# Kernel tuning notes

Hardware: AMD Instinct MI355X
Metric: run time of the kernel (lower is better)

## Reference

```python
import jax, jax.numpy as jnp
import numpy as np

N, T, K, C, O = 2048, 20, 32, 32, 64  # agents, timesteps, neighbors, in_ch, out_ch


def setup_inputs() -> dict:
    key = jax.random.key(0)
    ks = jax.random.split(key, 8)
    s = 0.05
    x = jax.random.normal(ks[0], (N, T, C), dtype=jnp.float32)
    A = jax.random.randint(ks[1], (T, N, K), 0, N)  # neighbor indices into agent dim
    conv_w = jax.random.normal(ks[2], (O, C), jnp.float32) * s  # 1x1 conv == linear [O,C]
    conv_b = jax.random.normal(ks[3], (O,), jnp.float32) * s
    w_ih = jax.random.normal(ks[4], (4 * O, O), jnp.float32) * s  # LSTM gates i,f,g,o
    w_hh = jax.random.normal(ks[5], (4 * O, O), jnp.float32) * s
    b_ih = jax.random.normal(ks[6], (4 * O,), jnp.float32) * s
    b_hh = jax.random.normal(ks[7], (4 * O,), jnp.float32) * s
    return dict(x=x, A=A, conv_w=conv_w, conv_b=conv_b,
                w_ih=w_ih, w_hh=w_hh, b_ih=b_ih, b_hh=b_hh)


def reference(x, A, conv_w, conv_b, w_ih, w_hh, b_ih, b_hh):
    n = x.shape[0]
    xt = jnp.transpose(x, (1, 0, 2))  # [T, N, C]
    # align == 1: per-timestep neighbor gather and relative difference
    gathered = jax.vmap(lambda xs, idx: xs[idx])(xt, A)  # [T, N, K, C]
    diff = gathered - xt[:, :, None, :]  # [T, N, K, C]
    # 1x1 conv (pointwise linear over channels)
    y = jnp.einsum('tnkc,oc->tnko', diff, conv_w) + conv_b  # [T, N, K, O]
    # AdaptiveMaxPool2d((seq_len, 1)): max over the neighbor axis K
    feat = jnp.max(y, axis=2)  # [T, N, O] -- LSTM input (time-major)

    h0 = jnp.zeros((n, O), jnp.float32)
    c0 = jnp.zeros((n, O), jnp.float32)

    def step(carry, x_t):
        h, c = carry
        g = x_t @ w_ih.T + h @ w_hh.T + (b_ih + b_hh)  # [N, 4O]
        i_g, f_g, g_g, o_g = jnp.split(g, 4, axis=-1)
        c = jax.nn.sigmoid(f_g) * c + jax.nn.sigmoid(i_g) * jnp.tanh(g_g)
        h = jax.nn.sigmoid(o_g) * jnp.tanh(c)
        return (h, c), h

    (hN, cN), hs = jax.lax.scan(step, (h0, c0), feat)
    out = jnp.transpose(hs, (1, 0, 2))  # [N, T, O]
    # state_tuple permuted to batch-first as in the torch module
    return out, hN[:, None, :], cN[:, None, :]
```

## Files before the change

kernel.cpp:

```cpp
#include <hip/hip_runtime.h>
#include <hip/hip_bf16.h>
#include <math.h>

#define NA 2048
#define TT 20
#define KK 32
#define CC 32
#define OO 64
#define GG 256

typedef __attribute__((ext_vector_type(8))) short short8;
typedef __attribute__((ext_vector_type(4))) float float4v;

__device__ __forceinline__ float fast_rcp(float x) {
    return __builtin_amdgcn_rcpf(x);
}
__device__ __forceinline__ float sigm(float x) {
    return fast_rcp(1.f + __expf(-x));
}
__device__ __forceinline__ float tanh_fast(float x) {
    return 1.f - 2.f * fast_rcp(1.f + __expf(2.f * x));
}
__device__ __forceinline__ unsigned cvt_rne(float f) {
    unsigned u = __float_as_uint(f);
    return (u + 0x7FFFu + ((u >> 16) & 1u)) >> 16;
}
__device__ __forceinline__ unsigned pack2(float a, float b) {
    return cvt_rne(a) | (cvt_rne(b) << 16);
}
__device__ __forceinline__ float bf_lo(unsigned u) {
    return __uint_as_float(u << 16);
}
__device__ __forceinline__ float bf_hi(unsigned u) {
    return __uint_as_float(u & 0xffff0000u);
}

__global__ __launch_bounds__(256) void proj_kernel(
    const float* __restrict__ x, const float* __restrict__ conv_w,
    const float* __restrict__ conv_b, const float* __restrict__ w_ih,
    const float* __restrict__ w_hh, const float* __restrict__ b_ih,
    const float* __restrict__ b_hh,
    __hip_bfloat16* __restrict__ P, unsigned short* __restrict__ wihb,
    unsigned short* __restrict__ whhb, float* __restrict__ biasT)
{
    const int tid = threadIdx.x;
    if (blockIdx.x == 0) {
        for (int e = tid; e < 4 * OO * OO; e += 256) {
            wihb[e] = (unsigned short)cvt_rne(w_ih[e]);
            whhb[e] = (unsigned short)cvt_rne(w_hh[e]);
        }
        float bj = b_ih[tid] + b_hh[tid];
        #pragma unroll
        for (int o = 0; o < OO; o += 4) {
            float4 cb = *(const float4*)(conv_b + o);
            float4 wr = *(const float4*)(w_ih + (size_t)tid * OO + o);
            bj = fmaf(cb.x, wr.x, bj); bj = fmaf(cb.y, wr.y, bj);
            bj = fmaf(cb.z, wr.z, bj); bj = fmaf(cb.w, wr.w, bj);
        }
        biasT[tid] = bj;
        return;
    }
    const int lane = tid & 63;
    const int wv = tid >> 6;
    float w[CC];
    #pragma unroll
    for (int c = 0; c < CC; c += 4) {
        float4 v = *(const float4*)(conv_w + lane * CC + c);
        w[c] = v.x; w[c + 1] = v.y; w[c + 2] = v.z; w[c + 3] = v.w;
    }
    const int rbase = (blockIdx.x - 1) * 16 + wv * 4;
    #pragma unroll
    for (int i = 0; i < 4; ++i) {
        int r = rbase + i;
        const float* xr = x + (size_t)r * CC;
        float a0 = 0.f, a1 = 0.f;
        #pragma unroll
        for (int c = 0; c < CC; c += 8) {
            float4 v = *(const float4*)(xr + c);
            float4 u = *(const float4*)(xr + c + 4);
            a0 = fmaf(v.x, w[c], a0);     a0 = fmaf(v.y, w[c + 1], a0);
            a0 = fmaf(v.z, w[c + 2], a0); a0 = fmaf(v.w, w[c + 3], a0);
            a1 = fmaf(u.x, w[c + 4], a1); a1 = fmaf(u.y, w[c + 5], a1);
            a1 = fmaf(u.z, w[c + 6], a1); a1 = fmaf(u.w, w[c + 7], a1);
        }
        int n = r / TT;
        int t = r - n * TT;
        ((unsigned short*)P)[(((size_t)t << 11) + n) * OO + lane] =
            (unsigned short)cvt_rne(a0 + a1);
    }
}

__global__ __launch_bounds__(256, 4) void gather_kernel(
    const __hip_bfloat16* __restrict__ P, const int* __restrict__ A,
    unsigned* __restrict__ featw)
{
    __shared__ int A_sh[4][128];
    const int tid = threadIdx.x;
    const int lane = tid & 63;
    const int wv = tid >> 6;
    const int bs = (blockIdx.x & 7) * 320 + (blockIdx.x >> 3);
    const int r0 = bs << 4;
    const int t = r0 >> 11;
    const unsigned short* Pt = (const unsigned short*)P + ((size_t)t << 17);

    const int rw = r0 + wv * 4;
    ((int2*)A_sh[wv])[lane] = ((const int2*)(A + ((size_t)rw << 5)))[lane];

    const int i_row = lane >> 4;
    const int oc8 = lane & 15;
    const char* plane = (const char*)Pt + oc8 * 8;
    const int* myA = &A_sh[wv][i_row * 32];

    const int nself = (rw + i_row) & (NA - 1);
    const uint2 su = *(const uint2*)(plane + ((size_t)nself << 7));

    float m0 = -INFINITY, m1 = -INFINITY, m2 = -INFINITY, m3 = -INFINITY;
    #pragma unroll
    for (int bb = 0; bb < 2; ++bb) {
        int idx[16];
        #pragma unroll
        for (int g = 0; g < 16; ++g)
            idx[g] = myA[bb * 16 + g];
        uint2 uv[16];
        #pragma unroll
        for (int g = 0; g < 16; ++g)
            uv[g] = *(const uint2*)(plane + ((size_t)idx[g] << 7));
        #pragma unroll
        for (int g = 0; g < 16; ++g) {
            m0 = fmaxf(m0, bf_lo(uv[g].x)); m1 = fmaxf(m1, bf_hi(uv[g].x));
            m2 = fmaxf(m2, bf_lo(uv[g].y)); m3 = fmaxf(m3, bf_hi(uv[g].y));
        }
    }
    uint2 pk;
    pk.x = pack2(m0 - bf_lo(su.x), m1 - bf_hi(su.x));
    pk.y = pack2(m2 - bf_lo(su.y), m3 - bf_hi(su.y));
    *(uint2*)&featw[((size_t)(rw + i_row) << 5) + oc8 * 2] = pk;
}

__global__ __launch_bounds__(256, 2) void lstm_kernel(
    const unsigned short* __restrict__ feat,
    const unsigned short* __restrict__ wihb,
    const unsigned short* __restrict__ whhb,
    const float* __restrict__ biasT, float* __restrict__ out)
{
    const int tid = threadIdx.x;
    const int lane = tid & 63;
    const int wv = tid >> 6;
    const int l15 = lane & 15;
    const int q = lane >> 4;
    const int a0 = blockIdx.x * 16;
    const int a = tid >> 4;
    const int c0 = (tid & 15) * 4;

    short8 bfI[4][2], bfH[4][2];
    #pragma unroll
    for (int tt2 = 0; tt2 < 4; ++tt2) {
        int row = wv * 64 + tt2 * 16 + l15;
        #pragma unroll
        for (int ks = 0; ks < 2; ++ks) {
            bfI[tt2][ks] =
                *(const short8*)(wihb + ((size_t)row << 6) + ks * 32 + q * 8);
            bfH[tt2][ks] =
                *(const short8*)(whhb + ((size_t)row << 6) + ks * 32 + q * 8);
        }
    }
    float4 bias4[4];
    #pragma unroll
    for (int g = 0; g < 4; ++g)
        bias4[g] = *(const float4*)(biasT + g * 64 + c0);

    __shared__ __align__(16) unsigned short h_sh[16 * 72];
    __shared__ float gp[4][16][68];

    {
        uint2 z; z.x = 0u; z.y = 0u;
        *(uint2*)&h_sh[a * 72 + c0] = z;
    }
    float cst[4] = {0.f, 0.f, 0.f, 0.f};

    short8 ff[2];
    #pragma unroll
    for (int ks = 0; ks < 2; ++ks)
        ff[ks] = *(const short8*)(
            feat + (((size_t)a0 + l15) << 6) + ks * 32 + q * 8);

    for (int t = 0; t < TT; ++t) {
        __syncthreads();

        float4v acc[4] = {{0.f, 0.f, 0.f, 0.f}, {0.f, 0.f, 0.f, 0.f},
                          {0.f, 0.f, 0.f, 0.f}, {0.f, 0.f, 0.f, 0.f}};
        #pragma unroll
        for (int ks = 0; ks < 2; ++ks) {
            short8 ah = *(const short8*)(&h_sh[l15 * 72 + ks * 32 + q * 8]);
            #pragma unroll
            for (int tt2 = 0; tt2 < 4; ++tt2) {
                acc[tt2] = __builtin_amdgcn_mfma_f32_16x16x32_bf16(
                    ff[ks], bfI[tt2][ks], acc[tt2], 0, 0, 0);
                acc[tt2] = __builtin_amdgcn_mfma_f32_16x16x32_bf16(
                    ah, bfH[tt2][ks], acc[tt2], 0, 0, 0);
            }
        }
        #pragma unroll
        for (int tt2 = 0; tt2 < 4; ++tt2)
            #pragma unroll
            for (int rg = 0; rg < 4; ++rg)
                gp[wv][q * 4 + rg][tt2 * 16 + l15] = acc[tt2][rg];

        short8 ffn[2];
        int tn = (t + 1 < TT) ? t + 1 : t;
        #pragma unroll
        for (int ks = 0; ks < 2; ++ks)
            ffn[ks] = *(const short8*)(
                feat + ((((size_t)tn << 11) + a0 + l15) << 6) + ks * 32 + q * 8);
        __syncthreads();

        float4 gv0 = *(const float4*)&gp[0][a][c0];
        float4 gv1 = *(const float4*)&gp[1][a][c0];
        float4 gv2 = *(const float4*)&gp[2][a][c0];
        float4 gv3 = *(const float4*)&gp[3][a][c0];
        float hv[4];
        {
            float gi[4] = {gv0.x + bias4[0].x, gv0.y + bias4[0].y,
                           gv0.z + bias4[0].z, gv0.w + bias4[0].w};
            float gf[4] = {gv1.x + bias4[1].x, gv1.y + bias4[1].y,
                           gv1.z + bias4[1].z, gv1.w + bias4[1].w};
            float gz[4] = {gv2.x + bias4[2].x, gv2.y + bias4[2].y,
                           gv2.z + bias4[2].z, gv2.w + bias4[2].w};
            float go[4] = {gv3.x + bias4[3].x, gv3.y + bias4[3].y,
                           gv3.z + bias4[3].z, gv3.w + bias4[3].w};
            #pragma unroll
            for (int e = 0; e < 4; ++e) {
                float ig = sigm(gi[e]);
                float fg = sigm(gf[e]);
                float zg = tanh_fast(gz[e]);
                float og = sigm(go[e]);
                cst[e] = fmaf(fg, cst[e], ig * zg);
                hv[e] = og * tanh_fast(cst[e]);
            }
        }
        {
            uint2 pk;
            pk.x = pack2(hv[0], hv[1]);
            pk.y = pack2(hv[2], hv[3]);
            *(uint2*)&h_sh[a * 72 + c0] = pk;
        }
        float4 ho; ho.x = hv[0]; ho.y = hv[1]; ho.z = hv[2]; ho.w = hv[3];
        *(float4*)(out + (((size_t)(a0 + a) * TT + t) << 6) + c0) = ho;
        if (t == TT - 1) {
            size_t hb = (size_t)NA * TT * OO;
            *(float4*)(out + hb + ((size_t)(a0 + a) << 6) + c0) = ho;
            float4 co; co.x = cst[0]; co.y = cst[1]; co.z = cst[2]; co.w = cst[3];
            *(float4*)(out + hb + ((size_t)NA << 6) + ((size_t)(a0 + a) << 6) + c0) = co;
        }
        ff[0] = ffn[0]; ff[1] = ffn[1];
    }
}

extern "C" void kernel_launch(void* const* d_in, const int* in_sizes, int n_in,
                              void* d_out, int out_size, void* d_ws, size_t ws_size,
                              hipStream_t stream) {
    const float* x      = (const float*)d_in[0];
    const int*   A      = (const int*)  d_in[1];
    const float* conv_w = (const float*)d_in[2];
    const float* conv_b = (const float*)d_in[3];
    const float* w_ih   = (const float*)d_in[4];
    const float* w_hh   = (const float*)d_in[5];
    const float* b_ih   = (const float*)d_in[6];
    const float* b_hh   = (const float*)d_in[7];
    float* out = (float*)d_out;

    char* ws = (char*)d_ws;
    __hip_bfloat16* P  = (__hip_bfloat16*)ws;
    size_t offF = (size_t)TT * NA * OO * 2;
    unsigned* featw = (unsigned*)(ws + offF);
    size_t offW = offF + (size_t)TT * NA * OO * 2;
    unsigned short* wihb = (unsigned short*)(ws + offW);
    unsigned short* whhb = wihb + 4 * OO * OO;
    float* biasT = (float*)(whhb + 4 * OO * OO);

    hipLaunchKernelGGL(proj_kernel, dim3(NA * TT / 16 + 1), dim3(256), 0, stream,
                       x, conv_w, conv_b, w_ih, w_hh, b_ih, b_hh,
                       P, wihb, whhb, biasT);
    hipLaunchKernelGGL(gather_kernel, dim3(NA * TT / 16), dim3(256), 0, stream,
                       P, A, featw);
    hipLaunchKernelGGL(lstm_kernel, dim3(NA / 16), dim3(256), 0, stream,
                       (const unsigned short*)featw, wihb, whhb, biasT, out);
}
```

Measured before the change: 129.0 us.

## Fuse neighbor gather-max into LSTM kernel with software-pipelined prefetch

Removes the separate gather kernel and its feature buffer: the LSTM kernel now gathers neighbor projections for step t+1 while computing step t, with features and neighbor indices double-buffered in shared memory. This avoids one launch and a global write and read of the feature tensor. The cost is that the gather work now runs on only 128 blocks instead of 2560, so it may extend the serial LSTM loop if its latency is not hidden, and register pressure rises.

New measurement: 149.3 us. 15.8% more time.

```diff
diff --git a/kernel.cpp b/kernel.cpp
--- a/kernel.cpp
+++ b/kernel.cpp
@@ -90,55 +90,8 @@
     }
 }
 
-__global__ __launch_bounds__(256, 4) void gather_kernel(
+__global__ __launch_bounds__(256, 2) void lstm_fused_kernel(
     const __hip_bfloat16* __restrict__ P, const int* __restrict__ A,
-    unsigned* __restrict__ featw)
-{
-    __shared__ int A_sh[4][128];
-    const int tid = threadIdx.x;
-    const int lane = tid & 63;
-    const int wv = tid >> 6;
-    const int bs = (blockIdx.x & 7) * 320 + (blockIdx.x >> 3);
-    const int r0 = bs << 4;
-    const int t = r0 >> 11;
-    const unsigned short* Pt = (const unsigned short*)P + ((size_t)t << 17);
-
-    const int rw = r0 + wv * 4;
-    ((int2*)A_sh[wv])[lane] = ((const int2*)(A + ((size_t)rw << 5)))[lane];
-
-    const int i_row = lane >> 4;
-    const int oc8 = lane & 15;
-    const char* plane = (const char*)Pt + oc8 * 8;
-    const int* myA = &A_sh[wv][i_row * 32];
-
-    const int nself = (rw + i_row) & (NA - 1);
-    const uint2 su = *(const uint2*)(plane + ((size_t)nself << 7));
-
-    float m0 = -INFINITY, m1 = -INFINITY, m2 = -INFINITY, m3 = -INFINITY;
-    #pragma unroll
-    for (int bb = 0; bb < 2; ++bb) {
-        int idx[16];
-        #pragma unroll
-        for (int g = 0; g < 16; ++g)
-            idx[g] = myA[bb * 16 + g];
-        uint2 uv[16];
-        #pragma unroll
-        for (int g = 0; g < 16; ++g)
-            uv[g] = *(const uint2*)(plane + ((size_t)idx[g] << 7));
-        #pragma unroll
-        for (int g = 0; g < 16; ++g) {
-            m0 = fmaxf(m0, bf_lo(uv[g].x)); m1 = fmaxf(m1, bf_hi(uv[g].x));
-            m2 = fmaxf(m2, bf_lo(uv[g].y)); m3 = fmaxf(m3, bf_hi(uv[g].y));
-        }
-    }
-    uint2 pk;
-    pk.x = pack2(m0 - bf_lo(su.x), m1 - bf_hi(su.x));
-    pk.y = pack2(m2 - bf_lo(su.y), m3 - bf_hi(su.y));
-    *(uint2*)&featw[((size_t)(rw + i_row) << 5) + oc8 * 2] = pk;
-}
-
-__global__ __launch_bounds__(256, 2) void lstm_kernel(
-    const unsigned short* __restrict__ feat,
     const unsigned short* __restrict__ wihb,
     const unsigned short* __restrict__ whhb,
     const float* __restrict__ biasT, float* __restrict__ out)
@@ -151,6 +104,7 @@
     const int a0 = blockIdx.x * 16;
     const int a = tid >> 4;
     const int c0 = (tid & 15) * 4;
+    const int oc8 = tid & 15;
 
     short8 bfI[4][2], bfH[4][2];
     #pragma unroll
@@ -171,6 +125,13 @@
 
     __shared__ __align__(16) unsigned short h_sh[16 * 72];
     __shared__ float gp[4][16][68];
+    __shared__ int A_sh[2][16 * KK];
+    __shared__ __align__(16) unsigned short feat_sh[2][16][72];
+
+    #pragma unroll
+    for (int b = 0; b < 2; ++b)
+        ((int2*)A_sh[b])[tid] =
+            ((const int2*)(A + ((size_t)b * NA + a0) * KK))[tid];
 
     {
         uint2 z; z.x = 0u; z.y = 0u;
@@ -178,24 +139,71 @@
     }
     float cst[4] = {0.f, 0.f, 0.f, 0.f};
 
-    short8 ff[2];
-    #pragma unroll
-    for (int ks = 0; ks < 2; ++ks)
-        ff[ks] = *(const short8*)(
-            feat + (((size_t)a0 + l15) << 6) + ks * 32 + q * 8);
+    __syncthreads();
+
+    const unsigned short* Pb = (const unsigned short*)P;
+
+    {
+        const char* plane = (const char*)Pb + oc8 * 8;
+        const int* myA = &A_sh[0][a * KK];
+        float m0 = -INFINITY, m1 = -INFINITY, m2 = -INFINITY, m3 = -INFINITY;
+        #pragma unroll
+        for (int bb = 0; bb < 2; ++bb) {
+            int idx[16];
+            #pragma unroll
+            for (int g = 0; g < 16; ++g)
+                idx[g] = myA[bb * 16 + g];
+            uint2 uv[16];
+            #pragma unroll
+            for (int g = 0; g < 16; ++g)
+                uv[g] = *(const uint2*)(plane + ((size_t)idx[g] << 7));
+            #pragma unroll
+            for (int g = 0; g < 16; ++g) {
+                m0 = fmaxf(m0, bf_lo(uv[g].x)); m1 = fmaxf(m1, bf_hi(uv[g].x));
+                m2 = fmaxf(m2, bf_lo(uv[g].y)); m3 = fmaxf(m3, bf_hi(uv[g].y));
+            }
+        }
+        uint2 su = *(const uint2*)(plane + ((size_t)(a0 + a) << 7));
+        uint2 pk;
+        pk.x = pack2(m0 - bf_lo(su.x), m1 - bf_hi(su.x));
+        pk.y = pack2(m2 - bf_lo(su.y), m3 - bf_hi(su.y));
+        *(uint2*)&feat_sh[0][a][oc8 * 4] = pk;
+    }
 
     for (int t = 0; t < TT; ++t) {
         __syncthreads();
 
+        const int tg = (t + 1 < TT) ? t + 1 : TT - 1;
+        const char* plane =
+            (const char*)(Pb + ((size_t)tg << 17)) + oc8 * 8;
+        const int* myA = &A_sh[(t + 1) & 1][a * KK];
+        int idx1[16], idx2[16];
+        #pragma unroll
+        for (int g = 0; g < 16; ++g) idx1[g] = myA[g];
+        #pragma unroll
+        for (int g = 0; g < 16; ++g) idx2[g] = myA[16 + g];
+        uint2 uv1[16], uv2[16];
+        #pragma unroll
+        for (int g = 0; g < 16; ++g)
+            uv1[g] = *(const uint2*)(plane + ((size_t)idx1[g] << 7));
+        #pragma unroll
+        for (int g = 0; g < 16; ++g)
+            uv2[g] = *(const uint2*)(plane + ((size_t)idx2[g] << 7));
+        uint2 su = *(const uint2*)(plane + ((size_t)(a0 + a) << 7));
+        const int ts = (t + 2 < TT) ? t + 2 : TT - 1;
+        int2 av = ((const int2*)(A + ((size_t)ts * NA + a0) * KK))[tid];
+
         float4v acc[4] = {{0.f, 0.f, 0.f, 0.f}, {0.f, 0.f, 0.f, 0.f},
                           {0.f, 0.f, 0.f, 0.f}, {0.f, 0.f, 0.f, 0.f}};
         #pragma unroll
         for (int ks = 0; ks < 2; ++ks) {
+            short8 ffk =
+                *(const short8*)&feat_sh[t & 1][l15][ks * 32 + q * 8];
             short8 ah = *(const short8*)(&h_sh[l15 * 72 + ks * 32 + q * 8]);
             #pragma unroll
             for (int tt2 = 0; tt2 < 4; ++tt2) {
                 acc[tt2] = __builtin_amdgcn_mfma_f32_16x16x32_bf16(
-                    ff[ks], bfI[tt2][ks], acc[tt2], 0, 0, 0);
+                    ffk, bfI[tt2][ks], acc[tt2], 0, 0, 0);
                 acc[tt2] = __builtin_amdgcn_mfma_f32_16x16x32_bf16(
                     ah, bfH[tt2][ks], acc[tt2], 0, 0, 0);
             }
@@ -206,12 +214,14 @@
             for (int rg = 0; rg < 4; ++rg)
                 gp[wv][q * 4 + rg][tt2 * 16 + l15] = acc[tt2][rg];
 
-        short8 ffn[2];
-        int tn = (t + 1 < TT) ? t + 1 : t;
-        #pragma unroll
-        for (int ks = 0; ks < 2; ++ks)
-            ffn[ks] = *(const short8*)(
-                feat + ((((size_t)tn << 11) + a0 + l15) << 6) + ks * 32 + q * 8);
+        ((int2*)A_sh[t & 1])[tid] = av;
+
+        float m0 = -INFINITY, m1 = -INFINITY, m2 = -INFINITY, m3 = -INFINITY;
+        #pragma unroll
+        for (int g = 0; g < 16; ++g) {
+            m0 = fmaxf(m0, bf_lo(uv1[g].x)); m1 = fmaxf(m1, bf_hi(uv1[g].x));
+            m2 = fmaxf(m2, bf_lo(uv1[g].y)); m3 = fmaxf(m3, bf_hi(uv1[g].y));
+        }
         __syncthreads();
 
         float4 gv0 = *(const float4*)&gp[0][a][c0];
@@ -252,7 +262,16 @@
             float4 co; co.x = cst[0]; co.y = cst[1]; co.z = cst[2]; co.w = cst[3];
             *(float4*)(out + hb + ((size_t)NA << 6) + ((size_t)(a0 + a) << 6) + c0) = co;
         }
-        ff[0] = ffn[0]; ff[1] = ffn[1];
+
+        #pragma unroll
+        for (int g = 0; g < 16; ++g) {
+            m0 = fmaxf(m0, bf_lo(uv2[g].x)); m1 = fmaxf(m1, bf_hi(uv2[g].x));
+            m2 = fmaxf(m2, bf_lo(uv2[g].y)); m3 = fmaxf(m3, bf_hi(uv2[g].y));
+        }
+        uint2 pk;
+        pk.x = pack2(m0 - bf_lo(su.x), m1 - bf_hi(su.x));
+        pk.y = pack2(m2 - bf_lo(su.y), m3 - bf_hi(su.y));
+        *(uint2*)&feat_sh[(t + 1) & 1][a][oc8 * 4] = pk;
     }
 }
 
@@ -271,9 +290,7 @@
 
     char* ws = (char*)d_ws;
     __hip_bfloat16* P  = (__hip_bfloat16*)ws;
-    size_t offF = (size_t)TT * NA * OO * 2;
-    unsigned* featw = (unsigned*)(ws + offF);
-    size_t offW = offF + (size_t)TT * NA * OO * 2;
+    size_t offW = (size_t)TT * NA * OO * 2;
     unsigned short* wihb = (unsigned short*)(ws + offW);
     unsigned short* whhb = wihb + 4 * OO * OO;
     float* biasT = (float*)(whhb + 4 * OO * OO);
@@ -281,8 +298,6 @@
     hipLaunchKernelGGL(proj_kernel, dim3(NA * TT / 16 + 1), dim3(256), 0, stream,
                        x, conv_w, conv_b, w_ih, w_hh, b_ih, b_hh,
                        P, wihb, whhb, biasT);
-    hipLaunchKernelGGL(gather_kernel, dim3(NA * TT / 16), dim3(256), 0, stream,
-                       P, A, featw);
-    hipLaunchKernelGGL(lstm_kernel, dim3(NA / 16), dim3(256), 0, stream,
-                       (const unsigned short*)featw, wihb, whhb, biasT, out);
-}
+    hipLaunchKernelGGL(lstm_fused_kernel, dim3(NA / 16), dim3(256), 0, stream,
+                       P, A, wihb, whhb, biasT, out);
+}
```

## Compute LSTM gates per-wave in registers, drop gate LDS round-trip

Applied to the files above, without the earlier changes.

Each wave now owns 16 output channels across all four gates, so the i/f/g/o accumulators for one channel sit in the same lane. The cell update then runs directly from the MFMA results instead of going through shared memory, which removes the gp staging array and one barrier per timestep. The h state is double-buffered in shared memory, leaving a single sync per step. Stores to out become scalar 4-byte writes with a 64-channel stride pattern instead of float4, which may cost store efficiency. The occupancy hint in launch_bounds is also dropped.

Result: no change. 130.2 us (median of 2 runs) (+1.0%).

```diff
diff --git a/kernel.cpp b/kernel.cpp
--- a/kernel.cpp
+++ b/kernel.cpp
@@ -137,7 +137,7 @@
     *(uint2*)&featw[((size_t)(rw + i_row) << 5) + oc8 * 2] = pk;
 }
 
-__global__ __launch_bounds__(256, 2) void lstm_kernel(
+__global__ __launch_bounds__(256) void lstm_kernel(
     const unsigned short* __restrict__ feat,
     const unsigned short* __restrict__ wihb,
     const unsigned short* __restrict__ whhb,
@@ -149,33 +149,30 @@
     const int l15 = lane & 15;
     const int q = lane >> 4;
     const int a0 = blockIdx.x * 16;
-    const int a = tid >> 4;
-    const int c0 = (tid & 15) * 4;
+    const int ch = wv * 16 + l15;
 
     short8 bfI[4][2], bfH[4][2];
     #pragma unroll
-    for (int tt2 = 0; tt2 < 4; ++tt2) {
-        int row = wv * 64 + tt2 * 16 + l15;
+    for (int g = 0; g < 4; ++g) {
+        int row = g * 64 + ch;
         #pragma unroll
         for (int ks = 0; ks < 2; ++ks) {
-            bfI[tt2][ks] =
+            bfI[g][ks] =
                 *(const short8*)(wihb + ((size_t)row << 6) + ks * 32 + q * 8);
-            bfH[tt2][ks] =
+            bfH[g][ks] =
                 *(const short8*)(whhb + ((size_t)row << 6) + ks * 32 + q * 8);
         }
     }
-    float4 bias4[4];
+    float bias_g[4];
     #pragma unroll
     for (int g = 0; g < 4; ++g)
-        bias4[g] = *(const float4*)(biasT + g * 64 + c0);
-
-    __shared__ __align__(16) unsigned short h_sh[16 * 72];
-    __shared__ float gp[4][16][68];
-
-    {
-        uint2 z; z.x = 0u; z.y = 0u;
-        *(uint2*)&h_sh[a * 72 + c0] = z;
-    }
+        bias_g[g] = biasT[g * 64 + ch];
+
+    __shared__ __align__(16) unsigned short h_sh[2][16 * 72];
+
+    for (int e = tid; e < 16 * 72 / 2; e += 256)
+        ((unsigned*)h_sh[0])[e] = 0u;
+
     float cst[4] = {0.f, 0.f, 0.f, 0.f};
 
     short8 ff[2];
@@ -184,27 +181,27 @@
         ff[ks] = *(const short8*)(
             feat + (((size_t)a0 + l15) << 6) + ks * 32 + q * 8);
 
+    __syncthreads();
+
     for (int t = 0; t < TT; ++t) {
-        __syncthreads();
+        short8 ah[2];
+        #pragma unroll
+        for (int ks = 0; ks < 2; ++ks)
+            ah[ks] = *(const short8*)(
+                &h_sh[t & 1][l15 * 72 + ks * 32 + q * 8]);
 
         float4v acc[4] = {{0.f, 0.f, 0.f, 0.f}, {0.f, 0.f, 0.f, 0.f},
                           {0.f, 0.f, 0.f, 0.f}, {0.f, 0.f, 0.f, 0.f}};
         #pragma unroll
         for (int ks = 0; ks < 2; ++ks) {
-            short8 ah = *(const short8*)(&h_sh[l15 * 72 + ks * 32 + q * 8]);
             #pragma unroll
-            for (int tt2 = 0; tt2 < 4; ++tt2) {
-                acc[tt2] = __builtin_amdgcn_mfma_f32_16x16x32_bf16(
-                    ff[ks], bfI[tt2][ks], acc[tt2], 0, 0, 0);
-                acc[tt2] = __builtin_amdgcn_mfma_f32_16x16x32_bf16(
-                    ah, bfH[tt2][ks], acc[tt2], 0, 0, 0);
+            for (int g = 0; g < 4; ++g) {
+                acc[g] = __builtin_amdgcn_mfma_f32_16x16x32_bf16(
+                    ff[ks], bfI[g][ks], acc[g], 0, 0, 0);
+                acc[g] = __builtin_amdgcn_mfma_f32_16x16x32_bf16(
+                    ah[ks], bfH[g][ks], acc[g], 0, 0, 0);
             }
         }
-        #pragma unroll
-        for (int tt2 = 0; tt2 < 4; ++tt2)
-            #pragma unroll
-            for (int rg = 0; rg < 4; ++rg)
-                gp[wv][q * 4 + rg][tt2 * 16 + l15] = acc[tt2][rg];
 
         short8 ffn[2];
         int tn = (t + 1 < TT) ? t + 1 : t;
@@ -212,46 +209,30 @@
         for (int ks = 0; ks < 2; ++ks)
             ffn[ks] = *(const short8*)(
                 feat + ((((size_t)tn << 11) + a0 + l15) << 6) + ks * 32 + q * 8);
+
+        #pragma unroll
+        for (int rg = 0; rg < 4; ++rg) {
+            float gi = acc[0][rg] + bias_g[0];
+            float gf = acc[1][rg] + bias_g[1];
+            float gz = acc[2][rg] + bias_g[2];
+            float go = acc[3][rg] + bias_g[3];
+            float ig = sigm(gi);
+            float fg = sigm(gf);
+            float zg = tanh_fast(gz);
+            float og = sigm(go);
+            cst[rg] = fmaf(fg, cst[rg], ig * zg);
+            float hv = og * tanh_fast(cst[rg]);
+            int agent = q * 4 + rg;
+            h_sh[(t + 1) & 1][agent * 72 + ch] = (unsigned short)cvt_rne(hv);
+            out[(((size_t)(a0 + agent) * TT + t) << 6) + ch] = hv;
+            if (t == TT - 1) {
+                size_t hb = (size_t)NA * TT * OO;
+                out[hb + ((size_t)(a0 + agent) << 6) + ch] = hv;
+                out[hb + ((size_t)NA << 6) + ((size_t)(a0 + agent) << 6) + ch] =
+                    cst[rg];
+            }
+        }
         __syncthreads();
-
-        float4 gv0 = *(const float4*)&gp[0][a][c0];
-        float4 gv1 = *(const float4*)&gp[1][a][c0];
-        float4 gv2 = *(const float4*)&gp[2][a][c0];
-        float4 gv3 = *(const float4*)&gp[3][a][c0];
-        float hv[4];
-        {
-            float gi[4] = {gv0.x + bias4[0].x, gv0.y + bias4[0].y,
-                           gv0.z + bias4[0].z, gv0.w + bias4[0].w};
-            float gf[4] = {gv1.x + bias4[1].x, gv1.y + bias4[1].y,
-                           gv1.z + bias4[1].z, gv1.w + bias4[1].w};
-            float gz[4] = {gv2.x + bias4[2].x, gv2.y + bias4[2].y,
-                           gv2.z + bias4[2].z, gv2.w + bias4[2].w};
-            float go[4] = {gv3.x + bias4[3].x, gv3.y + bias4[3].y,
-                           gv3.z + bias4[3].z, gv3.w + bias4[3].w};
-            #pragma unroll
-            for (int e = 0; e < 4; ++e) {
-                float ig = sigm(gi[e]);
-                float fg = sigm(gf[e]);
-                float zg = tanh_fast(gz[e]);
-                float og = sigm(go[e]);
-                cst[e] = fmaf(fg, cst[e], ig * zg);
-                hv[e] = og * tanh_fast(cst[e]);
-            }
-        }
-        {
-            uint2 pk;
-            pk.x = pack2(hv[0], hv[1]);
-            pk.y = pack2(hv[2], hv[3]);
-            *(uint2*)&h_sh[a * 72 + c0] = pk;
-        }
-        float4 ho; ho.x = hv[0]; ho.y = hv[1]; ho.z = hv[2]; ho.w = hv[3];
-        *(float4*)(out + (((size_t)(a0 + a) * TT + t) << 6) + c0) = ho;
-        if (t == TT - 1) {
-            size_t hb = (size_t)NA * TT * OO;
-            *(float4*)(out + hb + ((size_t)(a0 + a) << 6) + c0) = ho;
-            float4 co; co.x = cst[0]; co.y = cst[1]; co.z = cst[2]; co.w = cst[3];
-            *(float4*)(out + hb + ((size_t)NA << 6) + ((size_t)(a0 + a) << 6) + c0) = co;
-        }
         ff[0] = ffn[0]; ff[1] = ffn[1];
     }
 }
```
